# Optimization experiments

Measured on AMD Instinct MI355X. Metric: run time of the kernel, lower is better.

Reference implementation:

```python
import jax, jax.numpy as jnp
import numpy as np

N = 131072      # nodes
E = 2097152     # edges (avg in-degree ~16)
H = 128         # hidden_dim
OUT = 128       # out_dim
G = 8192        # number of graphs in batch
A = 28          # num_atom_type
L = 4           # layers


def setup_inputs() -> dict:
    key = jax.random.key(0)
    ks = jax.random.split(key, 12)
    h = jax.random.uniform(ks[0], (N, A), dtype=jnp.float32)
    src = jax.random.randint(ks[1], (E,), 0, N, dtype=jnp.int32)
    dst = jax.random.randint(ks[2], (E,), 0, N, dtype=jnp.int32)
    graph_id = jnp.sort(jax.random.randint(ks[3], (N,), 0, G, dtype=jnp.int32))
    # snorm_n = 1/sqrt(|V_g|) per node (graph_norm)
    gcnt = jax.ops.segment_sum(jnp.ones((N,), jnp.float32), graph_id, num_segments=G)
    snorm_n = (1.0 / jnp.sqrt(jnp.maximum(gcnt, 1.0)))[graph_id][:, None]
    # parameters (Bayesian linears treated as sampled fixed weights)
    W_emb = jax.random.normal(ks[4], (A, H), jnp.float32) / np.sqrt(A)
    W_node = jax.random.normal(ks[5], (L, 2 * H, H), jnp.float32) / np.sqrt(2 * H)
    b_node = jnp.zeros((L, H), jnp.float32)
    W_ro = jax.random.normal(ks[6], (H, OUT), jnp.float32) / np.sqrt(H)
    W_pred = jax.random.normal(ks[7], (OUT, 1), jnp.float32) / np.sqrt(OUT)
    b_pred = jnp.zeros((1,), jnp.float32)
    return {"h": h, "snorm_n": snorm_n, "W_emb": W_emb, "W_node": W_node,
            "b_node": b_node, "W_ro": W_ro, "W_pred": W_pred, "b_pred": b_pred,
            "src": src, "dst": dst, "graph_id": graph_id}


def reference(h, snorm_n, W_emb, W_node, b_node, W_ro, W_pred, b_pred, src, dst, graph_id):
    # in-degree for mean aggregation (constant per graph)
    deg = jax.ops.segment_sum(jnp.ones((E,), h.dtype), dst, num_segments=N)
    inv_deg = (1.0 / jnp.maximum(deg, 1.0))[:, None]
    # per-graph node counts for mean readout
    gcnt = jax.ops.segment_sum(jnp.ones((N,), h.dtype), graph_id, num_segments=G)
    inv_gcnt = (1.0 / jnp.maximum(gcnt, 1.0))[:, None]

    h = h @ W_emb  # input embedding (dropout = identity in eval)
    for l in range(L):
        h_in = h
        # mean aggregation of in-neighbor features: c[v] = mean_{u->v} h[u]
        c = jax.ops.segment_sum(h[src], dst, num_segments=N) * inv_deg
        # NodeApply: relu(Linear([h || c]))
        h = jax.nn.relu(jnp.concatenate([h, c], axis=1) @ W_node[l] + b_node[l])
        h = h * snorm_n          # graph_norm
        h = h + h_in             # residual
    h = h @ W_ro                 # linear_ro (no bias)
    hg = jax.ops.segment_sum(h, graph_id, num_segments=G) * inv_gcnt  # mean readout
    return hg @ W_pred + b_pred  # linear_predict -> [G, 1]
```

## Files before the change

kernel.cpp:

```cpp
#include <hip/hip_runtime.h>

constexpr int NN  = 131072;
constexpr int NE  = 2097152;
constexpr int HD  = 128;
constexpr int NG  = 8192;
constexpr int NA  = 28;
constexpr int NL  = 4;

constexpr int NB   = 256;
constexpr int BSH  = 9;
constexpr int BNOD = 512;
constexpr int CAP  = 10240;

constexpr size_t SZ_FB   = (size_t)NN * HD * 2;
constexpr size_t OFF_XB   = 0;
constexpr size_t OFF_YB   = OFF_XB + SZ_FB;
constexpr size_t OFF_PB   = OFF_YB + SZ_FB;
constexpr size_t OFF_ESRC = OFF_PB + SZ_FB;
constexpr size_t OFF_DEG  = OFF_ESRC + (size_t)NE * 4;
constexpr size_t OFF_GCNT = OFF_DEG + (size_t)NN * 4;
constexpr size_t OFF_ROW  = OFF_GCNT + (size_t)NG * 4;
constexpr size_t OFF_IDEG = OFF_ROW + (size_t)NN * 4;
constexpr size_t OFF_IGC  = OFF_IDEG + (size_t)NN * 4;
constexpr size_t OFF_BSUM = OFF_IGC + (size_t)NG * 4;
constexpr size_t OFF_COFF = OFF_BSUM + 512;
constexpr size_t OFF_WC   = OFF_COFF + 512;
constexpr size_t OFF_WNT  = OFF_WC + 512;
constexpr size_t OFF_EBUF = OFF_WNT + (size_t)NL * HD * 256 * 2;
constexpr size_t OFF_GCUR = OFF_EBUF + (size_t)NB * CAP * 4;
constexpr size_t OFF_WET  = OFF_GCUR + (size_t)NB * 4;

__device__ __forceinline__ float blo(uint x) { return __uint_as_float(x << 16); }
__device__ __forceinline__ float bhi(uint x) { return __uint_as_float(x & 0xFFFF0000u); }
__device__ __forceinline__ unsigned short f2b(float f) {
  uint u = __float_as_uint(f);
  return (unsigned short)((u + 0x7FFFu + ((u >> 16) & 1u)) >> 16);
}
__device__ __forceinline__ uint pack2(float a, float b) {
  uint ua = __float_as_uint(a), ub = __float_as_uint(b);
  uint lo = (ua + 0x7FFFu + ((ua >> 16) & 1u)) >> 16;
  uint hi = (ub + 0x7FFFu + ((ub >> 16) & 1u)) & 0xFFFF0000u;
  return lo | hi;
}

typedef __attribute__((ext_vector_type(8))) short bf16x8;
typedef __attribute__((ext_vector_type(4))) float f32x4;
typedef __attribute__((ext_vector_type(2))) float f32x2;

__device__ __forceinline__ uint pk_fp8x4(float a, float b, float c, float d) {
  int p = __builtin_amdgcn_cvt_pk_fp8_f32(a, b, 0, false);
  p = __builtin_amdgcn_cvt_pk_fp8_f32(c, d, p, true);
  return (uint)p;
}

__global__ void k_binit(int* __restrict__ gcur) {
  int b = threadIdx.x;
  gcur[b] = b * CAP;
}

__global__ __launch_bounds__(256) void k_bin(const int* __restrict__ src,
                                             const int* __restrict__ dst,
                                             int* __restrict__ gcur,
                                             uint* __restrict__ ebuf) {
  __shared__ int cnt[NB];
  __shared__ int gbase[NB];
  int t = threadIdx.x;
  cnt[t] = 0;
  int es[16], ed[16];
  int base = blockIdx.x * 4096 + t;
#pragma unroll
  for (int j = 0; j < 16; j++) {
    es[j] = src[base + j * 256];
    ed[j] = dst[base + j * 256];
  }
  __syncthreads();
#pragma unroll
  for (int j = 0; j < 16; j++) atomicAdd(&cnt[ed[j] >> BSH], 1);
  __syncthreads();
  int c = cnt[t];
  if (c > 0) gbase[t] = atomicAdd(&gcur[t], c);
  cnt[t] = 0;
  __syncthreads();
#pragma unroll
  for (int j = 0; j < 16; j++) {
    int b = ed[j] >> BSH;
    int r = atomicAdd(&cnt[b], 1);
    ebuf[(size_t)gbase[b] + r] = ((uint)(ed[j] & (BNOD - 1)) << 17) | (uint)es[j];
  }
}

__global__ __launch_bounds__(256) void k_deg(const int* __restrict__ gcur,
                                             const uint* __restrict__ ebuf,
                                             int* __restrict__ deg) {
  __shared__ int h[BNOD];
  int b = blockIdx.x, t = threadIdx.x;
  h[t] = 0; h[t + 256] = 0;
  int n = gcur[b] - b * CAP;
  __syncthreads();
  const uint* eb = ebuf + (size_t)b * CAP;
  for (int i = t; i < n; i += 256) atomicAdd(&h[eb[i] >> 17], 1);
  __syncthreads();
  deg[b * BNOD + t] = h[t];
  deg[b * BNOD + t + 256] = h[t + 256];
}

__global__ void k_scan1(const int* __restrict__ deg, int* __restrict__ bsum) {
  __shared__ int s[256];
  int b = blockIdx.x, t = threadIdx.x;
  const int4* p = (const int4*)(deg + (size_t)b * 1024);
  int4 v = p[t];
  s[t] = v.x + v.y + v.z + v.w;
  __syncthreads();
  for (int o = 128; o > 0; o >>= 1) {
    if (t < o) s[t] += s[t + o];
    __syncthreads();
  }
  if (t == 0) bsum[b] = s[0];
}

__global__ void k_scan2(const int* __restrict__ bsum, int* __restrict__ coff) {
  __shared__ int s[128];
  int t = threadIdx.x;
  int mine = bsum[t];
  s[t] = mine;
  __syncthreads();
  for (int o = 1; o < 128; o <<= 1) {
    int v = (t >= o) ? s[t - o] : 0;
    __syncthreads();
    s[t] += v;
    __syncthreads();
  }
  coff[t] = s[t] - mine;
}

__global__ void k_scan3(const int* __restrict__ deg, const int* __restrict__ coff,
                        int* __restrict__ row_start, float* __restrict__ inv_deg) {
  __shared__ int s[256];
  int b = blockIdx.x, t = threadIdx.x;
  int base = b * 1024 + t * 4;
  const int4* p = (const int4*)(deg + base);
  int4 d = *p;
  int lsum = d.x + d.y + d.z + d.w;
  s[t] = lsum;
  __syncthreads();
  for (int o = 1; o < 256; o <<= 1) {
    int v = (t >= o) ? s[t - o] : 0;
    __syncthreads();
    s[t] += v;
    __syncthreads();
  }
  int pre = coff[b] + s[t] - lsum;
  int r0 = pre, r1 = r0 + d.x, r2 = r1 + d.y, r3 = r2 + d.z;
  row_start[base] = r0;  row_start[base + 1] = r1;
  row_start[base + 2] = r2;  row_start[base + 3] = r3;
  inv_deg[base]     = 1.0f / fmaxf((float)d.x, 1.0f);
  inv_deg[base + 1] = 1.0f / fmaxf((float)d.y, 1.0f);
  inv_deg[base + 2] = 1.0f / fmaxf((float)d.z, 1.0f);
  inv_deg[base + 3] = 1.0f / fmaxf((float)d.w, 1.0f);
}

__global__ __launch_bounds__(256) void k_place2(const int* __restrict__ gcur,
                                                const uint* __restrict__ ebuf,
                                                const int* __restrict__ row_start,
                                                int* __restrict__ esrc) {
  __shared__ int cur[BNOD];
  int b = blockIdx.x, t = threadIdx.x;
  cur[t] = row_start[b * BNOD + t];
  cur[t + 256] = row_start[b * BNOD + t + 256];
  int n = gcur[b] - b * CAP;
  __syncthreads();
  const uint* eb = ebuf + (size_t)b * CAP;
  for (int i = t; i < n; i += 256) {
    uint p = eb[i];
    int r = atomicAdd(&cur[p >> 17], 1);
    esrc[r] = (int)(p & 0x1FFFFu);
  }
}

__global__ void k_ghist(const int* __restrict__ gid, int* __restrict__ gcnt) {
  int i = blockIdx.x * blockDim.x + threadIdx.x;
  if (i < NN) atomicAdd(&gcnt[gid[i]], 1);
}

__global__ void k_ginit(const int* __restrict__ gcnt, float* __restrict__ inv_gcnt,
                        float* __restrict__ out, const float* __restrict__ b_pred) {
  int g = blockIdx.x * blockDim.x + threadIdx.x;
  if (g < NG) {
    inv_gcnt[g] = 1.0f / fmaxf((float)gcnt[g], 1.0f);
    out[g] = b_pred[0];
  }
}

__global__ void k_wprep(const float* __restrict__ Wn, unsigned short* __restrict__ Wnt) {
  int i = blockIdx.x * 256 + threadIdx.x;
  int l = i >> 15;
  int k = (i >> 7) & 255;
  int c = i & 127;
  float v = Wn[((size_t)l * 256 + k) * HD + c];
  Wnt[((size_t)l * HD + c) * 256 + k] = f2b(v);
}

__global__ void k_weprep(const float* __restrict__ We, unsigned short* __restrict__ Wet) {
  int i = blockIdx.x * 256 + threadIdx.x;
  int col = i >> 5, k = i & 31;
  Wet[i] = (k < NA) ? f2b(We[(size_t)k * HD + col]) : (unsigned short)0;
}

__global__ __launch_bounds__(256) void k_embed(const float* __restrict__ h,
                                               const unsigned short* __restrict__ Wet,
                                               unsigned short* __restrict__ Xb) {
  int t = threadIdx.x;
  int lane = t & 63, w = t >> 6;
  int wr = w >> 1, wc = w & 1;
  int row0 = blockIdx.x * 64 + wr * 32;
  int col0 = wc * 64;
  int fr = lane & 15;
  int fk = (lane >> 4) * 8;

  f32x4 acc[2][4] = {};
  bf16x8 a[2];
#pragma unroll
  for (int rt = 0; rt < 2; rt++) {
    int row = row0 + rt * 16 + fr;
    const float* hp = h + (size_t)row * NA + fk;
    float4 p = *(const float4*)hp;
    float4 q = make_float4(0.f, 0.f, 0.f, 0.f);
    if (fk < 24) q = *(const float4*)(hp + 4);
    a[rt][0] = (short)f2b(p.x); a[rt][1] = (short)f2b(p.y);
    a[rt][2] = (short)f2b(p.z); a[rt][3] = (short)f2b(p.w);
    a[rt][4] = (short)f2b(q.x); a[rt][5] = (short)f2b(q.y);
    a[rt][6] = (short)f2b(q.z); a[rt][7] = (short)f2b(q.w);
  }
#pragma unroll
  for (int ct = 0; ct < 4; ct++) {
    int col = col0 + ct * 16 + fr;
    bf16x8 b = *(const bf16x8*)(Wet + (size_t)col * 32 + fk);
#pragma unroll
    for (int rt = 0; rt < 2; rt++)
      acc[rt][ct] = __builtin_amdgcn_mfma_f32_16x16x32_bf16(a[rt], b, acc[rt][ct], 0, 0, 0);
  }
  int oc = lane & 15, orb = (lane >> 4) * 4;
#pragma unroll
  for (int rt = 0; rt < 2; rt++) {
#pragma unroll
    for (int ct = 0; ct < 4; ct++) {
      int col = col0 + ct * 16 + oc;
#pragma unroll
      for (int r = 0; r < 4; r++) {
        int row = row0 + rt * 16 + orb + r;
        Xb[(size_t)row * HD + col] = f2b(acc[rt][ct][r]);
      }
    }
  }
}

__global__ __launch_bounds__(256) void k_pq(const unsigned short* __restrict__ Hb,
                                            uint* __restrict__ Pb8,
                                            unsigned short* __restrict__ Qb,
                                            const unsigned short* __restrict__ Wt,
                                            const float* __restrict__ bias) {
  int t = threadIdx.x;
  int lane = t & 63, w = t >> 6;
  int ng = w >> 1, cg = w & 1;
  int fr = lane & 15, fkg = lane >> 4;
  int n0 = blockIdx.x * 64 + ng * 32;

  f32x4 accQ[2][4] = {}, accP[2][4] = {};
#pragma unroll
  for (int ks = 0; ks < 4; ks++) {
    bf16x8 aH[2];
#pragma unroll
    for (int nt = 0; nt < 2; nt++)
      aH[nt] = *(const bf16x8*)(Hb + (size_t)(n0 + nt * 16 + fr) * HD + ks * 32 + fkg * 8);
#pragma unroll
    for (int ct = 0; ct < 4; ct++) {
      const unsigned short* wrow =
          Wt + (size_t)(cg * 64 + ct * 16 + fr) * 256 + ks * 32 + fkg * 8;
      bf16x8 b1 = *(const bf16x8*)wrow;
      bf16x8 b2 = *(const bf16x8*)(wrow + 128);
#pragma unroll
      for (int nt = 0; nt < 2; nt++) {
        accQ[nt][ct] = __builtin_amdgcn_mfma_f32_16x16x32_bf16(b1, aH[nt], accQ[nt][ct], 0, 0, 0);
        accP[nt][ct] = __builtin_amdgcn_mfma_f32_16x16x32_bf16(b2, aH[nt], accP[nt][ct], 0, 0, 0);
      }
    }
  }
#pragma unroll
  for (int nt = 0; nt < 2; nt++) {
    int node = n0 + nt * 16 + fr;
#pragma unroll
    for (int ct = 0; ct < 4; ct++) {
      int c0 = cg * 64 + ct * 16 + fkg * 4;
      float4 bv = *(const float4*)(bias + c0);
      uint2 q;
      q.x = pack2(accQ[nt][ct][0] + bv.x, accQ[nt][ct][1] + bv.y);
      q.y = pack2(accQ[nt][ct][2] + bv.z, accQ[nt][ct][3] + bv.w);
      *(uint2*)(Qb + (size_t)node * HD + c0) = q;
      Pb8[(size_t)node * 32 + (c0 >> 2)] =
          pk_fp8x4(accP[nt][ct][0], accP[nt][ct][1], accP[nt][ct][2], accP[nt][ct][3]);
    }
  }
}

__global__ __launch_bounds__(256) void k_gapply(const uint2* __restrict__ Pg,
                      const uint4* __restrict__ Qg, const uint4* __restrict__ Hres,
                      uint4* __restrict__ Og,
                      const int* __restrict__ row_start, const int* __restrict__ deg,
                      const int* __restrict__ esrc, const float* __restrict__ inv_deg,
                      const float* __restrict__ snorm,
                      const float* __restrict__ wcv, const int* __restrict__ gid,
                      const float* __restrict__ inv_gcnt, float* __restrict__ out,
                      int last) {
  int v = blockIdx.x * 4 + (threadIdx.x >> 6);
  int lane = threadIdx.x & 63;
  int eg = lane >> 4;
  int cl = lane & 15;
  int rs = __builtin_amdgcn_readfirstlane(row_start[v]);
  int d  = __builtin_amdgcn_readfirstlane(deg[v]);

  float id = inv_deg[v];
  float sn = snorm[v];
  uint4 q  = Qg[(size_t)v * 16 + cl];
  uint4 hr = Hres[(size_t)v * 16 + cl];

  int dcap = min(d, 64);
  int myidx = 0;
  if (lane < dcap) myidx = esrc[rs + lane];

  float a0 = 0.f, a1 = 0.f, a2 = 0.f, a3 = 0.f;
  float a4 = 0.f, a5 = 0.f, a6 = 0.f, a7 = 0.f;

#define ACCX(X)                                                             \
  { f32x2 p0 = __builtin_amdgcn_cvt_pk_f32_fp8((int)(X).x, false);          \
    f32x2 p1 = __builtin_amdgcn_cvt_pk_f32_fp8((int)(X).x, true);           \
    f32x2 p2 = __builtin_amdgcn_cvt_pk_f32_fp8((int)(X).y, false);          \
    f32x2 p3 = __builtin_amdgcn_cvt_pk_f32_fp8((int)(X).y, true);           \
    a0 += p0[0]; a1 += p0[1]; a2 += p1[0]; a3 += p1[1];                     \
    a4 += p2[0]; a5 += p2[1]; a6 += p3[0]; a7 += p3[1]; }

  int e = 0;
  for (; e + 8 <= dcap; e += 8) {
    int i0 = __shfl(myidx, e + eg, 64);
    int i1 = __shfl(myidx, e + 4 + eg, 64);
    uint2 x0 = Pg[(size_t)i0 * 16 + cl];
    uint2 x1 = Pg[(size_t)i1 * 16 + cl];
    ACCX(x0)
    ACCX(x1)
  }
  if (e + 4 <= dcap) {
    int i0 = __shfl(myidx, e + eg, 64);
    uint2 x = Pg[(size_t)i0 * 16 + cl];
    ACCX(x)
    e += 4;
  }
  if (e < dcap) {
    uint2 x = make_uint2(0u, 0u);
    if (e + eg < dcap) {
      int i0 = __shfl(myidx, e + eg, 64);
      x = Pg[(size_t)i0 * 16 + cl];
    }
    ACCX(x)
  }
  for (int ee = 64; ee < d; ee += 4) {
    uint2 x = make_uint2(0u, 0u);
    if (ee + eg < d) x = Pg[(size_t)esrc[rs + ee + eg] * 16 + cl];
    ACCX(x)
  }
#undef ACCX

  a0 += __shfl_xor(a0, 16, 64);  a0 += __shfl_xor(a0, 32, 64);
  a1 += __shfl_xor(a1, 16, 64);  a1 += __shfl_xor(a1, 32, 64);
  a2 += __shfl_xor(a2, 16, 64);  a2 += __shfl_xor(a2, 32, 64);
  a3 += __shfl_xor(a3, 16, 64);  a3 += __shfl_xor(a3, 32, 64);
  a4 += __shfl_xor(a4, 16, 64);  a4 += __shfl_xor(a4, 32, 64);
  a5 += __shfl_xor(a5, 16, 64);  a5 += __shfl_xor(a5, 32, 64);
  a6 += __shfl_xor(a6, 16, 64);  a6 += __shfl_xor(a6, 32, 64);
  a7 += __shfl_xor(a7, 16, 64);  a7 += __shfl_xor(a7, 32, 64);

  if (eg == 0) {
    float o0 = fmaxf(blo(q.x) + a0 * id, 0.f) * sn + blo(hr.x);
    float o1 = fmaxf(bhi(q.x) + a1 * id, 0.f) * sn + bhi(hr.x);
    float o2 = fmaxf(blo(q.y) + a2 * id, 0.f) * sn + blo(hr.y);
    float o3 = fmaxf(bhi(q.y) + a3 * id, 0.f) * sn + bhi(hr.y);
    float o4 = fmaxf(blo(q.z) + a4 * id, 0.f) * sn + blo(hr.z);
    float o5 = fmaxf(bhi(q.z) + a5 * id, 0.f) * sn + bhi(hr.z);
    float o6 = fmaxf(blo(q.w) + a6 * id, 0.f) * sn + blo(hr.w);
    float o7 = fmaxf(bhi(q.w) + a7 * id, 0.f) * sn + bhi(hr.w);
    if (!last) {
      uint4 o;
      o.x = pack2(o0, o1);
      o.y = pack2(o2, o3);
      o.z = pack2(o4, o5);
      o.w = pack2(o6, o7);
      Og[(size_t)v * 16 + cl] = o;
    } else {
      float4 w0 = *(const float4*)(wcv + 8 * cl);
      float4 w1 = *(const float4*)(wcv + 8 * cl + 4);
      float p = o0 * w0.x + o1 * w0.y + o2 * w0.z + o3 * w0.w
              + o4 * w1.x + o5 * w1.y + o6 * w1.z + o7 * w1.w;
      p += __shfl_xor(p, 8, 64);
      p += __shfl_xor(p, 4, 64);
      p += __shfl_xor(p, 2, 64);
      p += __shfl_xor(p, 1, 64);
      if (cl == 0) {
        int g = gid[v];
        atomicAdd(&out[g], p * inv_gcnt[g]);
      }
    }
  }
}

__global__ void k_wcombo(const float* __restrict__ W_ro, const float* __restrict__ W_pred,
                         float* __restrict__ wcv) {
  int i = threadIdx.x;
  float a = 0.f;
  for (int j = 0; j < HD; j++) a += W_ro[i * HD + j] * W_pred[j];
  wcv[i] = a;
}

extern "C" void kernel_launch(void* const* d_in, const int* in_sizes, int n_in,
                              void* d_out, int out_size, void* d_ws, size_t ws_size,
                              hipStream_t stream) {
  const float* h      = (const float*)d_in[0];
  const float* snorm  = (const float*)d_in[1];
  const float* W_emb  = (const float*)d_in[2];
  const float* W_node = (const float*)d_in[3];
  const float* b_node = (const float*)d_in[4];
  const float* W_ro   = (const float*)d_in[5];
  const float* W_pred = (const float*)d_in[6];
  const float* b_pred = (const float*)d_in[7];
  const int*   src    = (const int*)d_in[8];
  const int*   dst    = (const int*)d_in[9];
  const int*   gid    = (const int*)d_in[10];
  float* out = (float*)d_out;

  char* ws = (char*)d_ws;
  unsigned short* Xb   = (unsigned short*)(ws + OFF_XB);
  unsigned short* Yb   = (unsigned short*)(ws + OFF_YB);
  uint*  Pb8      = (uint*)(ws + OFF_PB);
  int*   esrc     = (int*)(ws + OFF_ESRC);
  int*   deg      = (int*)(ws + OFF_DEG);
  int*   gcnt     = (int*)(ws + OFF_GCNT);
  int*   row_s    = (int*)(ws + OFF_ROW);
  float* inv_deg  = (float*)(ws + OFF_IDEG);
  float* inv_gcnt = (float*)(ws + OFF_IGC);
  int*   bsum     = (int*)(ws + OFF_BSUM);
  int*   coff     = (int*)(ws + OFF_COFF);
  float* wcv      = (float*)(ws + OFF_WC);
  unsigned short* Wnt = (unsigned short*)(ws + OFF_WNT);
  uint*  ebuf     = (uint*)(ws + OFF_EBUF);
  int*   gcur     = (int*)(ws + OFF_GCUR);
  unsigned short* Wet = (unsigned short*)(ws + OFF_WET);

  hipMemsetAsync(ws + OFF_GCNT, 0, (size_t)NG * 4, stream);

  k_binit<<<1, NB, 0, stream>>>(gcur);
  k_bin<<<NE / 4096, 256, 0, stream>>>(src, dst, gcur, ebuf);
  k_deg<<<NB, 256, 0, stream>>>(gcur, ebuf, deg);
  k_scan1<<<NN / 1024, 256, 0, stream>>>(deg, bsum);
  k_scan2<<<1, 128, 0, stream>>>(bsum, coff);
  k_scan3<<<NN / 1024, 256, 0, stream>>>(deg, coff, row_s, inv_deg);
  k_place2<<<NB, 256, 0, stream>>>(gcur, ebuf, row_s, esrc);
  k_ghist<<<NN / 256, 256, 0, stream>>>(gid, gcnt);
  k_ginit<<<NG / 256, 256, 0, stream>>>(gcnt, inv_gcnt, out, b_pred);
  k_wprep<<<(NL * 256 * HD) / 256, 256, 0, stream>>>(W_node, Wnt);
  k_weprep<<<(HD * 32) / 256, 256, 0, stream>>>(W_emb, Wet);
  k_wcombo<<<1, 128, 0, stream>>>(W_ro, W_pred, wcv);

  k_embed<<<NN / 64, 256, 0, stream>>>(h, Wet, Xb);

  for (int l = 0; l < NL; l++) {
    unsigned short* hb = (l & 1) ? Yb : Xb;
    unsigned short* qo = (l & 1) ? Xb : Yb;
    k_pq<<<NN / 64, 256, 0, stream>>>(hb, Pb8, qo, Wnt + (size_t)l * HD * 256,
                                      b_node + (size_t)l * HD);
    k_gapply<<<NN / 4, 256, 0, stream>>>((const uint2*)Pb8, (const uint4*)qo,
                                         (const uint4*)hb, (uint4*)qo,
                                         row_s, deg, esrc, inv_deg, snorm,
                                         wcv, gid, inv_gcnt, out, (l == NL - 1) ? 1 : 0);
  }
}
```

Measured before the change: 562.0 us.

## Fuse CSR build into one kernel, merge prep kernels, unroll gather by 16

Replaces the deg/scan1/scan2/scan3/place2 chain with a single per-bucket CSR kernel. Each block redoes a 256-entry scan of the bucket counts to find its global offset, then histograms, scans and places its edges locally. The small weight and graph-count prep kernels are merged into one multi-role launch, cutting launch count from about 16 to 4 before the embed. The edge-gather loop in the aggregation kernel is unrolled to 16 edges per iteration so more independent loads are in flight, at the cost of higher register pressure.

Result: faster. 539.4 us (median of 2 runs) (-4.0%).

```diff
diff --git a/kernel.cpp b/kernel.cpp
--- a/kernel.cpp
+++ b/kernel.cpp
@@ -22,9 +22,7 @@
 constexpr size_t OFF_ROW  = OFF_GCNT + (size_t)NG * 4;
 constexpr size_t OFF_IDEG = OFF_ROW + (size_t)NN * 4;
 constexpr size_t OFF_IGC  = OFF_IDEG + (size_t)NN * 4;
-constexpr size_t OFF_BSUM = OFF_IGC + (size_t)NG * 4;
-constexpr size_t OFF_COFF = OFF_BSUM + 512;
-constexpr size_t OFF_WC   = OFF_COFF + 512;
+constexpr size_t OFF_WC   = OFF_IGC + (size_t)NG * 4;
 constexpr size_t OFF_WNT  = OFF_WC + 512;
 constexpr size_t OFF_EBUF = OFF_WNT + (size_t)NL * HD * 256 * 2;
 constexpr size_t OFF_GCUR = OFF_EBUF + (size_t)NB * CAP * 4;
@@ -53,9 +51,40 @@
   return (uint)p;
 }
 
-__global__ void k_binit(int* __restrict__ gcur) {
-  int b = threadIdx.x;
-  gcur[b] = b * CAP;
+__global__ void k_ghist(const int* __restrict__ gid, int* __restrict__ gcnt) {
+  int i = blockIdx.x * blockDim.x + threadIdx.x;
+  if (i < NN) atomicAdd(&gcnt[gid[i]], 1);
+}
+
+__global__ void k_prep(int* __restrict__ gcur, const int* __restrict__ gcnt,
+                       float* __restrict__ inv_gcnt, float* __restrict__ out,
+                       const float* __restrict__ b_pred,
+                       const float* __restrict__ Wn, unsigned short* __restrict__ Wnt,
+                       const float* __restrict__ We, unsigned short* __restrict__ Wet,
+                       const float* __restrict__ W_ro, const float* __restrict__ W_pred,
+                       float* __restrict__ wcv) {
+  int bi = blockIdx.x, t = threadIdx.x;
+  if (bi == 0) {
+    gcur[t] = t * CAP;
+  } else if (bi < 1 + NG / 256) {
+    int g = (bi - 1) * 256 + t;
+    inv_gcnt[g] = 1.0f / fmaxf((float)gcnt[g], 1.0f);
+    out[g] = b_pred[0];
+  } else if (bi < 1 + NG / 256 + 512) {
+    int i = (bi - 1 - NG / 256) * 256 + t;
+    int l = i >> 15, k = (i >> 7) & 255, c = i & 127;
+    Wnt[((size_t)l * HD + c) * 256 + k] = f2b(Wn[((size_t)l * 256 + k) * HD + c]);
+  } else if (bi < 1 + NG / 256 + 512 + 16) {
+    int i = (bi - 1 - NG / 256 - 512) * 256 + t;
+    int col = i >> 5, k = i & 31;
+    Wet[i] = (k < NA) ? f2b(We[(size_t)k * HD + col]) : (unsigned short)0;
+  } else {
+    if (t < 128) {
+      float a = 0.f;
+      for (int j = 0; j < HD; j++) a += W_ro[t * HD + j] * W_pred[j];
+      wcv[t] = a;
+    }
+  }
 }
 
 __global__ __launch_bounds__(256) void k_bin(const int* __restrict__ src,
@@ -89,121 +118,57 @@
   }
 }
 
-__global__ __launch_bounds__(256) void k_deg(const int* __restrict__ gcur,
+__global__ __launch_bounds__(256) void k_csr(const int* __restrict__ gcur,
                                              const uint* __restrict__ ebuf,
-                                             int* __restrict__ deg) {
+                                             int* __restrict__ deg,
+                                             int* __restrict__ row_start,
+                                             float* __restrict__ inv_deg,
+                                             int* __restrict__ esrc) {
   __shared__ int h[BNOD];
+  __shared__ int ps[NB];
+  __shared__ int bs[NB];
   int b = blockIdx.x, t = threadIdx.x;
+
+  bs[t] = gcur[t] - t * CAP;
   h[t] = 0; h[t + 256] = 0;
+  __syncthreads();
+  for (int o = 1; o < 256; o <<= 1) {
+    int v = (t >= o) ? bs[t - o] : 0;
+    __syncthreads();
+    bs[t] += v;
+    __syncthreads();
+  }
+  int boff = (b == 0) ? 0 : bs[b - 1];
   int n = gcur[b] - b * CAP;
-  __syncthreads();
+
   const uint* eb = ebuf + (size_t)b * CAP;
   for (int i = t; i < n; i += 256) atomicAdd(&h[eb[i] >> 17], 1);
   __syncthreads();
-  deg[b * BNOD + t] = h[t];
-  deg[b * BNOD + t + 256] = h[t + 256];
-}
-
-__global__ void k_scan1(const int* __restrict__ deg, int* __restrict__ bsum) {
-  __shared__ int s[256];
-  int b = blockIdx.x, t = threadIdx.x;
-  const int4* p = (const int4*)(deg + (size_t)b * 1024);
-  int4 v = p[t];
-  s[t] = v.x + v.y + v.z + v.w;
-  __syncthreads();
-  for (int o = 128; o > 0; o >>= 1) {
-    if (t < o) s[t] += s[t + o];
+
+  int d0 = h[2 * t], d1 = h[2 * t + 1];
+  ps[t] = d0 + d1;
+  __syncthreads();
+  for (int o = 1; o < 256; o <<= 1) {
+    int v = (t >= o) ? ps[t - o] : 0;
     __syncthreads();
-  }
-  if (t == 0) bsum[b] = s[0];
-}
-
-__global__ void k_scan2(const int* __restrict__ bsum, int* __restrict__ coff) {
-  __shared__ int s[128];
-  int t = threadIdx.x;
-  int mine = bsum[t];
-  s[t] = mine;
-  __syncthreads();
-  for (int o = 1; o < 128; o <<= 1) {
-    int v = (t >= o) ? s[t - o] : 0;
+    ps[t] += v;
     __syncthreads();
-    s[t] += v;
-    __syncthreads();
-  }
-  coff[t] = s[t] - mine;
-}
-
-__global__ void k_scan3(const int* __restrict__ deg, const int* __restrict__ coff,
-                        int* __restrict__ row_start, float* __restrict__ inv_deg) {
-  __shared__ int s[256];
-  int b = blockIdx.x, t = threadIdx.x;
-  int base = b * 1024 + t * 4;
-  const int4* p = (const int4*)(deg + base);
-  int4 d = *p;
-  int lsum = d.x + d.y + d.z + d.w;
-  s[t] = lsum;
-  __syncthreads();
-  for (int o = 1; o < 256; o <<= 1) {
-    int v = (t >= o) ? s[t - o] : 0;
-    __syncthreads();
-    s[t] += v;
-    __syncthreads();
-  }
-  int pre = coff[b] + s[t] - lsum;
-  int r0 = pre, r1 = r0 + d.x, r2 = r1 + d.y, r3 = r2 + d.z;
-  row_start[base] = r0;  row_start[base + 1] = r1;
-  row_start[base + 2] = r2;  row_start[base + 3] = r3;
-  inv_deg[base]     = 1.0f / fmaxf((float)d.x, 1.0f);
-  inv_deg[base + 1] = 1.0f / fmaxf((float)d.y, 1.0f);
-  inv_deg[base + 2] = 1.0f / fmaxf((float)d.z, 1.0f);
-  inv_deg[base + 3] = 1.0f / fmaxf((float)d.w, 1.0f);
-}
-
-__global__ __launch_bounds__(256) void k_place2(const int* __restrict__ gcur,
-                                                const uint* __restrict__ ebuf,
-                                                const int* __restrict__ row_start,
-                                                int* __restrict__ esrc) {
-  __shared__ int cur[BNOD];
-  int b = blockIdx.x, t = threadIdx.x;
-  cur[t] = row_start[b * BNOD + t];
-  cur[t + 256] = row_start[b * BNOD + t + 256];
-  int n = gcur[b] - b * CAP;
-  __syncthreads();
-  const uint* eb = ebuf + (size_t)b * CAP;
+  }
+  int excl = ps[t] - (d0 + d1);
+  int r0 = boff + excl, r1 = r0 + d0;
+  int v0 = b * BNOD + 2 * t;
+  deg[v0] = d0;  deg[v0 + 1] = d1;
+  row_start[v0] = r0;  row_start[v0 + 1] = r1;
+  inv_deg[v0]     = 1.0f / fmaxf((float)d0, 1.0f);
+  inv_deg[v0 + 1] = 1.0f / fmaxf((float)d1, 1.0f);
+  __syncthreads();
+  h[2 * t] = r0;  h[2 * t + 1] = r1;
+  __syncthreads();
   for (int i = t; i < n; i += 256) {
     uint p = eb[i];
-    int r = atomicAdd(&cur[p >> 17], 1);
+    int r = atomicAdd(&h[p >> 17], 1);
     esrc[r] = (int)(p & 0x1FFFFu);
   }
-}
-
-__global__ void k_ghist(const int* __restrict__ gid, int* __restrict__ gcnt) {
-  int i = blockIdx.x * blockDim.x + threadIdx.x;
-  if (i < NN) atomicAdd(&gcnt[gid[i]], 1);
-}
-
-__global__ void k_ginit(const int* __restrict__ gcnt, float* __restrict__ inv_gcnt,
-                        float* __restrict__ out, const float* __restrict__ b_pred) {
-  int g = blockIdx.x * blockDim.x + threadIdx.x;
-  if (g < NG) {
-    inv_gcnt[g] = 1.0f / fmaxf((float)gcnt[g], 1.0f);
-    out[g] = b_pred[0];
-  }
-}
-
-__global__ void k_wprep(const float* __restrict__ Wn, unsigned short* __restrict__ Wnt) {
-  int i = blockIdx.x * 256 + threadIdx.x;
-  int l = i >> 15;
-  int k = (i >> 7) & 255;
-  int c = i & 127;
-  float v = Wn[((size_t)l * 256 + k) * HD + c];
-  Wnt[((size_t)l * HD + c) * 256 + k] = f2b(v);
-}
-
-__global__ void k_weprep(const float* __restrict__ We, unsigned short* __restrict__ Wet) {
-  int i = blockIdx.x * 256 + threadIdx.x;
-  int col = i >> 5, k = i & 31;
-  Wet[i] = (k < NA) ? f2b(We[(size_t)k * HD + col]) : (unsigned short)0;
 }
 
 __global__ __launch_bounds__(256) void k_embed(const float* __restrict__ h,
@@ -339,13 +304,28 @@
     a4 += p2[0]; a5 += p2[1]; a6 += p3[0]; a7 += p3[1]; }
 
   int e = 0;
-  for (; e + 8 <= dcap; e += 8) {
+  for (; e + 16 <= dcap; e += 16) {
+    int i0 = __shfl(myidx, e + eg, 64);
+    int i1 = __shfl(myidx, e + 4 + eg, 64);
+    int i2 = __shfl(myidx, e + 8 + eg, 64);
+    int i3 = __shfl(myidx, e + 12 + eg, 64);
+    uint2 x0 = Pg[(size_t)i0 * 16 + cl];
+    uint2 x1 = Pg[(size_t)i1 * 16 + cl];
+    uint2 x2 = Pg[(size_t)i2 * 16 + cl];
+    uint2 x3 = Pg[(size_t)i3 * 16 + cl];
+    ACCX(x0)
+    ACCX(x1)
+    ACCX(x2)
+    ACCX(x3)
+  }
+  if (e + 8 <= dcap) {
     int i0 = __shfl(myidx, e + eg, 64);
     int i1 = __shfl(myidx, e + 4 + eg, 64);
     uint2 x0 = Pg[(size_t)i0 * 16 + cl];
     uint2 x1 = Pg[(size_t)i1 * 16 + cl];
     ACCX(x0)
     ACCX(x1)
+    e += 8;
   }
   if (e + 4 <= dcap) {
     int i0 = __shfl(myidx, e + eg, 64);
@@ -410,14 +390,6 @@
   }
 }
 
-__global__ void k_wcombo(const float* __restrict__ W_ro, const float* __restrict__ W_pred,
-                         float* __restrict__ wcv) {
-  int i = threadIdx.x;
-  float a = 0.f;
-  for (int j = 0; j < HD; j++) a += W_ro[i * HD + j] * W_pred[j];
-  wcv[i] = a;
-}
-
 extern "C" void kernel_launch(void* const* d_in, const int* in_sizes, int n_in,
                               void* d_out, int out_size, void* d_ws, size_t ws_size,
                               hipStream_t stream) {
@@ -444,8 +416,6 @@
   int*   row_s    = (int*)(ws + OFF_ROW);
   float* inv_deg  = (float*)(ws + OFF_IDEG);
   float* inv_gcnt = (float*)(ws + OFF_IGC);
-  int*   bsum     = (int*)(ws + OFF_BSUM);
-  int*   coff     = (int*)(ws + OFF_COFF);
   float* wcv      = (float*)(ws + OFF_WC);
   unsigned short* Wnt = (unsigned short*)(ws + OFF_WNT);
   uint*  ebuf     = (uint*)(ws + OFF_EBUF);
@@ -454,18 +424,11 @@
 
   hipMemsetAsync(ws + OFF_GCNT, 0, (size_t)NG * 4, stream);
 
-  k_binit<<<1, NB, 0, stream>>>(gcur);
+  k_ghist<<<NN / 256, 256, 0, stream>>>(gid, gcnt);
+  k_prep<<<1 + NG / 256 + 512 + 16 + 1, 256, 0, stream>>>(
+      gcur, gcnt, inv_gcnt, out, b_pred, W_node, Wnt, W_emb, Wet, W_ro, W_pred, wcv);
   k_bin<<<NE / 4096, 256, 0, stream>>>(src, dst, gcur, ebuf);
-  k_deg<<<NB, 256, 0, stream>>>(gcur, ebuf, deg);
-  k_scan1<<<NN / 1024, 256, 0, stream>>>(deg, bsum);
-  k_scan2<<<1, 128, 0, stream>>>(bsum, coff);
-  k_scan3<<<NN / 1024, 256, 0, stream>>>(deg, coff, row_s, inv_deg);
-  k_place2<<<NB, 256, 0, stream>>>(gcur, ebuf, row_s, esrc);
-  k_ghist<<<NN / 256, 256, 0, stream>>>(gid, gcnt);
-  k_ginit<<<NG / 256, 256, 0, stream>>>(gcnt, inv_gcnt, out, b_pred);
-  k_wprep<<<(NL * 256 * HD) / 256, 256, 0, stream>>>(W_node, Wnt);
-  k_weprep<<<(HD * 32) / 256, 256, 0, stream>>>(W_emb, Wet);
-  k_wcombo<<<1, 128, 0, stream>>>(W_ro, W_pred, wcv);
+  k_csr<<<NB, 256, 0, stream>>>(gcur, ebuf, deg, row_s, inv_deg, esrc);
 
   k_embed<<<NN / 64, 256, 0, stream>>>(h, Wet, Xb);
 
```
